# Performance work log

Hardware: AMD Instinct MI355X
Metric: run time of the kernel (lower is better)

## Reference

```python
import jax, jax.numpy as jnp
import numpy as np

TS = 0.1
ECNUM = 1024
CA1NUM = 1024
CA3NUM = 1024
CA3SIGMA = 5.0
TRACKLEN = 100
ACTNUM = 2
BS = 8192
CUELOC = int(0.1 * TRACKLEN)  # sensory cue injected at this step
NOISE_P = 0.04 * TS           # per-step EC3 spontaneous-spike probability


def _xavier_std(fan_in, fan_out):
    return float(np.sqrt(2.0 / (fan_in + fan_out)))


def setup_inputs() -> dict:
    key = jax.random.key(0)
    ks = jax.random.split(key, 6)
    cue = jax.random.normal(ks[0], (BS, ECNUM), jnp.float32)
    ec5_init = jax.random.uniform(ks[1], (BS, ECNUM), jnp.float32)
    wca3ca1 = jax.random.uniform(ks[2], (CA3NUM, CA1NUM), jnp.float32) * 0.01
    wec3ca1 = jax.random.normal(ks[3], (ECNUM, CA1NUM), jnp.float32) * _xavier_std(ECNUM, CA1NUM)
    wca1ec5 = jax.random.normal(ks[4], (CA1NUM, ECNUM), jnp.float32) * _xavier_std(CA1NUM, ECNUM)
    wca1act = jax.random.normal(ks[5], (CA1NUM, ACTNUM), jnp.float32) * _xavier_std(CA1NUM, ACTNUM)
    ca1bias = jnp.zeros((CA1NUM,), jnp.float32)
    ec5bias = jnp.zeros((ECNUM,), jnp.float32)
    actbias = jnp.zeros((ACTNUM,), jnp.float32)
    return {"cue": cue, "ec5_init": ec5_init, "wca3ca1": wca3ca1,
            "wec3ca1": wec3ca1, "wca1ec5": wca1ec5, "wca1act": wca1act,
            "ca1bias": ca1bias, "ec5bias": ec5bias, "actbias": actbias}


def _forward(cue, ec5_init, wca3ca1, wec3ca1, wca1ec5, wca1act, ca1bias, ec5bias, actbias):
    bs = cue.shape[0]
    dt = cue.dtype
    # CA3 place-cell tuning curves for all positions: (T, ca3num)
    ca3center = jnp.linspace(0.0, TRACKLEN, CA3NUM).astype(dt)
    xs = jnp.arange(TRACKLEN)
    ca3_all = jnp.exp(-((ca3center[None, :] - xs[:, None].astype(dt)) ** 2)
                      / (2.0 * CA3SIGMA ** 2))
    drive = ca3_all @ wca3ca1            # (T, ca1num), precomputed CA3->CA1 drive
    cue_mask = (xs == CUELOC).astype(dt)  # (T,)
    noise_key = jax.random.key(42)

    ec3_0 = jnp.zeros((bs, ECNUM), dt)
    ca1_0 = jnp.zeros((bs, CA1NUM), dt)

    def step(carry, inp):
        ec3, ec5, _ = carry
        d, m, t = inp
        ca1 = jax.nn.relu(d[None, :] * (1.0 + jax.nn.sigmoid(ec3 @ wec3ca1)) - ca1bias)
        ec5 = ec5 + (10.0 * TS) * (ca1 @ wca1ec5) + ec5bias
        ec5 = 0.5 + 0.5 * jax.nn.sigmoid(4.0 * (ec5 - 0.5))
        ec3 = ec5 * ec3 + m * cue
        k = jax.random.fold_in(noise_key, t)
        ec3 = ec3 + 0.2 * jax.random.bernoulli(k, NOISE_P, (bs, ECNUM)).astype(dt)
        return (ec3, ec5, ca1), None

    (ec3, ec5, ca1), _ = jax.lax.scan(step, (ec3_0, ec5_init, ca1_0),
                                      (drive, cue_mask, xs))
    return ca1 @ wca1act + actbias       # (bs, actnum)


def reference(cue, ec5_init, wca3ca1, wec3ca1, wca1ec5, wca1act, ca1bias, ec5bias, actbias):
    return _forward(cue, ec5_init, wca3ca1, wec3ca1, wca1ec5, wca1act,
                    ca1bias, ec5bias, actbias)
```

## Files before the change

### kernel.cpp

```cpp
#include <hip/hip_runtime.h>
#include <stdint.h>

#define BS 8192
#define NDIM 1024
#define T_STEPS 100
#define CUE_T 10
#define BK 64
#define NKT (NDIM / BK)

typedef __attribute__((ext_vector_type(8))) short bf16x8;
typedef __attribute__((ext_vector_type(16))) float f32x16;

__device__ inline uint16_t f32_to_bf16(float f) {
    uint32_t u = __float_as_uint(f);
    uint32_t r = u + 0x7fffu + ((u >> 16) & 1u);
    return (uint16_t)(r >> 16);
}
__device__ inline float bf16_to_f32(uint16_t h) {
    return __uint_as_float(((uint32_t)h) << 16);
}

__host__ __device__ inline uint32_t rotl32_(uint32_t x, uint32_t r) {
    return (x << r) | (x >> (32u - r));
}

__host__ __device__ inline void tf2x32(uint32_t k0, uint32_t k1,
                                       uint32_t x0, uint32_t x1,
                                       uint32_t &o0, uint32_t &o1) {
    uint32_t ks2 = k0 ^ k1 ^ 0x1BD11BDAu;
    x0 += k0; x1 += k1;
#define TF_R4(a,b,c,d) \
    x0 += x1; x1 = rotl32_(x1,(a)); x1 ^= x0; \
    x0 += x1; x1 = rotl32_(x1,(b)); x1 ^= x0; \
    x0 += x1; x1 = rotl32_(x1,(c)); x1 ^= x0; \
    x0 += x1; x1 = rotl32_(x1,(d)); x1 ^= x0;
    TF_R4(13,15,26,6)  x0 += k1;  x1 += ks2 + 1u;
    TF_R4(17,29,16,24) x0 += ks2; x1 += k0 + 2u;
    TF_R4(13,15,26,6)  x0 += k0;  x1 += k1 + 3u;
    TF_R4(17,29,16,24) x0 += k1;  x1 += ks2 + 4u;
    TF_R4(13,15,26,6)  x0 += ks2; x1 += k0 + 5u;
#undef TF_R4
    o0 = x0; o1 = x1;
}

__device__ __forceinline__ void tf2x32_x4_fold(uint32_t k0, uint32_t k1,
                                               const uint32_t idx[4],
                                               uint32_t bits[4]) {
    uint32_t ks2 = k0 ^ k1 ^ 0x1BD11BDAu;
    uint32_t x0[4], x1[4];
    #pragma unroll
    for (int i = 0; i < 4; ++i) { x0[i] = k0; x1[i] = idx[i] + k1; }
#define TF4_R(rot) \
    _Pragma("unroll") \
    for (int i = 0; i < 4; ++i) { \
        x0[i] += x1[i]; x1[i] = rotl32_(x1[i], (rot)); x1[i] ^= x0[i]; }
#define TF4_K(a0, a1) \
    _Pragma("unroll") \
    for (int i = 0; i < 4; ++i) { x0[i] += (a0); x1[i] += (a1); }
    TF4_R(13) TF4_R(15) TF4_R(26) TF4_R(6)  TF4_K(k1, ks2 + 1u)
    TF4_R(17) TF4_R(29) TF4_R(16) TF4_R(24) TF4_K(ks2, k0 + 2u)
    TF4_R(13) TF4_R(15) TF4_R(26) TF4_R(6)  TF4_K(k0, k1 + 3u)
    TF4_R(17) TF4_R(29) TF4_R(16) TF4_R(24) TF4_K(k1, ks2 + 4u)
    TF4_R(13) TF4_R(15) TF4_R(26) TF4_R(6)  TF4_K(ks2, k0 + 5u)
#undef TF4_R
#undef TF4_K
    #pragma unroll
    for (int i = 0; i < 4; ++i) bits[i] = x0[i] ^ x1[i];
}

__device__ inline float sigmoidf_(float x) {
    float e = __expf(-x);
    return __builtin_amdgcn_rcpf(1.0f + e);
}

__device__ __forceinline__ void gload16(const uint16_t* g, uint16_t* l) {
    __builtin_amdgcn_global_load_lds(
        (const __attribute__((address_space(1))) void*)g,
        (__attribute__((address_space(3))) void*)l, 16, 0, 0);
}

__global__ void init_kernel(const float* __restrict__ ec5_init,
                            uint16_t* __restrict__ ec3bf,
                            uint16_t* __restrict__ ec5bf, int n) {
    int i = blockIdx.x * blockDim.x + threadIdx.x;
    if (i < n) { ec3bf[i] = 0; ec5bf[i] = f32_to_bf16(ec5_init[i]); }
}

__global__ __launch_bounds__(256) void drive_kernel(const float* __restrict__ W,
                                                    float* __restrict__ drive) {
    __shared__ float g[4][1024];
    const int t0 = blockIdx.x * 4;
    const int c = blockIdx.y * 64 + (threadIdx.x & 63);
    const int tt = threadIdx.x >> 6;
    const float stepf = 100.0f / 1023.0f;
    for (int i = threadIdx.x; i < 4096; i += 256) {
        int t_ = i >> 10, j = i & 1023;
        float d = stepf * (float)j - (float)(t0 + t_);
        g[t_][j] = expf(-(d * d) * 0.02f);
    }
    __syncthreads();
    float a = 0.f;
    for (int j = 0; j < 1024; ++j)
        a = fmaf(g[tt][j], W[(size_t)j * NDIM + c], a);
    drive[(size_t)(t0 + tt) * NDIM + c] = a;
}

__global__ __launch_bounds__(256) void wtrans_kernel(const float* __restrict__ W,
                                                     uint16_t* __restrict__ Wt) {
    __shared__ float tile[32][33];
    int k0 = blockIdx.x * 32, n0 = blockIdx.y * 32;
    int tx = threadIdx.x & 31, ty = threadIdx.x >> 5;
    #pragma unroll
    for (int i = 0; i < 32; i += 8)
        tile[ty + i][tx] = W[(size_t)(k0 + ty + i) * NDIM + n0 + tx];
    __syncthreads();
    #pragma unroll
    for (int i = 0; i < 32; i += 8)
        Wt[(size_t)(n0 + ty + i) * NDIM + k0 + tx] = f32_to_bf16(tile[tx][ty + i]);
}

template<bool NOISE>
__device__ __forceinline__ void gemm_core_t(const uint16_t* __restrict__ A,
                                            const uint16_t* __restrict__ Bt,
                                            uint16_t* As, uint16_t* Bs,
                                            f32x16 acc[2][2],
                                            uint32_t k0_, uint32_t k1_,
                                            uint32_t obase, uint64_t &mask) {
    const int tid = threadIdx.x;
    const int wid = tid >> 6, lane = tid & 63;
    const int row0 = blockIdx.x * 128, col0 = blockIdx.y * 128;
    const int srow = lane >> 3;
    const int soff = ((lane & 7) ^ srow) * 8;
    const uint16_t* aS[4]; const uint16_t* bS[4];
    #pragma unroll
    for (int i = 0; i < 4; ++i) {
        int ch = wid * 4 + i;
        aS[i] = A  + (size_t)(row0 + ch * 8 + srow) * NDIM + soff;
        bS[i] = Bt + (size_t)(col0 + ch * 8 + srow) * NDIM + soff;
    }
    const int l31 = lane & 31, l5 = lane >> 5;
    const int wr = wid >> 1, wc = wid & 1;
    int aoff[2][4], boff[2][4];
    #pragma unroll
    for (int m = 0; m < 2; ++m)
        #pragma unroll
        for (int kk = 0; kk < 4; ++kk) {
            int ar = wr * 64 + m * 32 + l31;
            aoff[m][kk] = ar * BK + ((((kk << 1) | l5) ^ (ar & 7)) << 3);
            int br = wc * 64 + m * 32 + l31;
            boff[m][kk] = br * BK + ((((kk << 1) | l5) ^ (br & 7)) << 3);
        }

    #pragma unroll
    for (int i = 0; i < 4; ++i) {
        int ch = wid * 4 + i;
        gload16(aS[i], As + ch * 512);
        gload16(bS[i], Bs + ch * 512);
    }

    for (int kt = 0; kt < NKT; ++kt) {
        const int cur = kt & 1;
        if (kt + 1 < NKT) {
            const int nb = (cur ^ 1) * 8192;
            const int k0n = (kt + 1) * BK;
            #pragma unroll
            for (int i = 0; i < 4; ++i) {
                int ch = wid * 4 + i;
                gload16(aS[i] + k0n, As + nb + ch * 512);
                gload16(bS[i] + k0n, Bs + nb + ch * 512);
            }
            asm volatile("s_waitcnt vmcnt(8)" ::: "memory");
        } else {
            asm volatile("s_waitcnt vmcnt(0)" ::: "memory");
        }
        __builtin_amdgcn_s_barrier();
        __builtin_amdgcn_sched_barrier(0);
        const uint16_t* as = As + cur * 8192;
        const uint16_t* bs = Bs + cur * 8192;
        bf16x8 af[2][4], bfr[2][4];
        #pragma unroll
        for (int m = 0; m < 2; ++m)
            #pragma unroll
            for (int kk = 0; kk < 4; ++kk) {
                af[m][kk]  = *(const bf16x8*)&as[aoff[m][kk]];
                bfr[m][kk] = *(const bf16x8*)&bs[boff[m][kk]];
            }
        #pragma unroll
        for (int kk = 0; kk < 4; ++kk)
            #pragma unroll
            for (int m = 0; m < 2; ++m)
                #pragma unroll
                for (int n = 0; n < 2; ++n)
                    acc[m][n] = __builtin_amdgcn_mfma_f32_32x32x16_bf16(
                        af[m][kk], bfr[n][kk], acc[m][n], 0, 0, 0);
        if (NOISE) {
            uint32_t idx[4], bits[4];
            const uint32_t base = obase + (uint32_t)((kt >> 1) << 14)
                                + (uint32_t)((kt & 1) << 2);
            #pragma unroll
            for (int u = 0; u < 4; ++u) idx[u] = base + u;
            tf2x32_x4_fold(k0_, k1_, idx, bits);
            #pragma unroll
            for (int u = 0; u < 4; ++u) {
                float uu = __uint_as_float((bits[u] >> 9) | 0x3f800000u) - 1.0f;
                mask |= (uint64_t)(uu < 0.004f ? 1u : 0u) << ((kt << 2) + u);
            }
        }
        __builtin_amdgcn_sched_barrier(0);
        __builtin_amdgcn_s_barrier();
    }
}

__device__ __forceinline__ void acc_to_lds(float* lacc, f32x16 acc[2][2]) {
    const int tid = threadIdx.x, wid = tid >> 6, lane = tid & 63;
    const int wr = wid >> 1, wc = wid & 1, l31 = lane & 31, l5 = lane >> 5;
    #pragma unroll
    for (int m = 0; m < 2; ++m)
        #pragma unroll
        for (int n = 0; n < 2; ++n) {
            int c = wc * 64 + n * 32 + l31;
            int chunk = c >> 2, cj = c & 3;
            #pragma unroll
            for (int e = 0; e < 16; ++e) {
                int r = wr * 64 + m * 32 + (e & 3) + ((e >> 2) << 3) + (l5 << 2);
                lacc[r * 128 + ((chunk ^ (r & 31)) << 2) + cj] = acc[m][n][e];
            }
        }
}

__device__ __forceinline__ void acc_read8(const float* lacc, int r, int a,
                                          float4 &v0, float4 &v1) {
    int rb = r & 31;
    v0 = *(const float4*)&lacc[r * 128 + ((((a << 1) | 0) ^ rb) << 2)];
    v1 = *(const float4*)&lacc[r * 128 + ((((a << 1) | 1) ^ rb) << 2)];
}

__global__ __launch_bounds__(256, 2) void gemm1_kernel(
    const uint16_t* __restrict__ ec3bf, const uint16_t* __restrict__ W1t,
    const float* __restrict__ drv, const float* __restrict__ bias,
    uint16_t* __restrict__ ca1bf, float* __restrict__ ca1f, int writef32,
    uint64_t* __restrict__ maskbuf, uint32_t k0_, uint32_t k1_)
{
    __shared__ __align__(16) uint16_t SM[2][16384];
    uint16_t* As = SM[0];
    uint16_t* Bs = SM[1];
    f32x16 acc[2][2];
    #pragma unroll
    for (int m = 0; m < 2; ++m)
        #pragma unroll
        for (int n = 0; n < 2; ++n)
            acc[m][n] = (f32x16)(0.0f);

    const int tid = threadIdx.x;
    const int row0 = blockIdx.x * 128, col0 = blockIdx.y * 128;
    const int a = tid & 15;
    const uint32_t obase = (uint32_t)(row0 + (tid >> 4)) * NDIM
                         + (uint32_t)(col0 + a * 8);
    uint64_t mask = 0;
    gemm_core_t<true>(ec3bf, W1t, As, Bs, acc, k0_, k1_, obase, mask);

    maskbuf[(size_t)(blockIdx.y * 64 + blockIdx.x) * 256 + tid] = mask;

    float* lacc = (float*)SM;
    acc_to_lds(lacc, acc);
    __syncthreads();

    #pragma unroll
    for (int i = 0; i < 8; ++i) {
        int r = (tid >> 4) + i * 16;
        float4 v0, v1;
        acc_read8(lacc, r, a, v0, v1);
        int gc = col0 + a * 8;
        float4 d0 = *(const float4*)&drv[gc];
        float4 d1 = *(const float4*)&drv[gc + 4];
        float4 b0 = *(const float4*)&bias[gc];
        float4 b1 = *(const float4*)&bias[gc + 4];
        size_t off = (size_t)(row0 + r) * NDIM + gc;
        float vout[8];
        #pragma unroll
        for (int j = 0; j < 8; ++j) {
            float accv = j < 4 ? v0[j] : v1[j - 4];
            float dv = j < 4 ? d0[j] : d1[j - 4];
            float bi = j < 4 ? b0[j] : b1[j - 4];
            float s = sigmoidf_(accv);
            float v = dv * (1.0f + s) - bi;
            vout[j] = v > 0.0f ? v : 0.0f;
        }
        bf16x8 pk;
        #pragma unroll
        for (int j = 0; j < 8; ++j) pk[j] = (short)f32_to_bf16(vout[j]);
        *(bf16x8*)&ca1bf[off] = pk;
        if (writef32) {
            float4 f0 = {vout[0], vout[1], vout[2], vout[3]};
            float4 f1 = {vout[4], vout[5], vout[6], vout[7]};
            *(float4*)&ca1f[off] = f0;
            *(float4*)&ca1f[off + 4] = f1;
        }
    }
}

__global__ __launch_bounds__(256, 2) void gemm2_kernel(
    const uint16_t* __restrict__ ca1bf, const uint16_t* __restrict__ W2t,
    const float* __restrict__ cue, const float* __restrict__ bias,
    uint16_t* __restrict__ ec3bf, uint16_t* __restrict__ ec5bf,
    const uint64_t* __restrict__ maskbuf, int inject)
{
    __shared__ __align__(16) uint16_t SM[2][16384];
    uint16_t* As = SM[0];
    uint16_t* Bs = SM[1];
    f32x16 acc[2][2];
    #pragma unroll
    for (int m = 0; m < 2; ++m)
        #pragma unroll
        for (int n = 0; n < 2; ++n)
            acc[m][n] = (f32x16)(0.0f);

    const int tid = threadIdx.x;
    const int row0 = blockIdx.x * 128, col0 = blockIdx.y * 128;
    const int a = tid & 15;
    const uint64_t mask = maskbuf[(size_t)(blockIdx.y * 64 + blockIdx.x) * 256 + tid];

    uint64_t dummy = 0;
    gemm_core_t<false>(ca1bf, W2t, As, Bs, acc, 0u, 0u, 0u, dummy);

    bf16x8 e3v[8], e5v[8];
    #pragma unroll
    for (int i = 0; i < 8; ++i) {
        size_t off = (size_t)(row0 + (tid >> 4) + i * 16) * NDIM + col0 + a * 8;
        e3v[i] = *(const bf16x8*)&ec3bf[off];
        e5v[i] = *(const bf16x8*)&ec5bf[off];
    }

    float* lacc = (float*)SM;
    acc_to_lds(lacc, acc);
    __syncthreads();

    #pragma unroll
    for (int i = 0; i < 8; ++i) {
        int r = (tid >> 4) + i * 16;
        float4 v0, v1;
        acc_read8(lacc, r, a, v0, v1);
        int gc = col0 + a * 8;
        size_t off = (size_t)(row0 + r) * NDIM + gc;
        float4 b0 = *(const float4*)&bias[gc];
        float4 b1 = *(const float4*)&bias[gc + 4];
        float4 c0 = {0.f,0.f,0.f,0.f}, c1 = {0.f,0.f,0.f,0.f};
        if (inject) {
            c0 = *(const float4*)&cue[off];
            c1 = *(const float4*)&cue[off + 4];
        }
        bf16x8 p3, p5;
        #pragma unroll
        for (int j = 0; j < 8; ++j) {
            float accv = j < 4 ? v0[j] : v1[j - 4];
            float bi = j < 4 ? b0[j] : b1[j - 4];
            float e5 = bf16_to_f32((uint16_t)e5v[i][j]);
            float e3 = bf16_to_f32((uint16_t)e3v[i][j]);
            float u = e5 + accv + bi;
            float e5n = 0.5f + 0.5f * sigmoidf_(4.0f * (u - 0.5f));
            float e3n = e5n * e3;
            if (inject) e3n += (j < 4 ? c0[j] : c1[j - 4]);
            e3n += ((mask >> (i * 8 + j)) & 1ull) ? 0.2f : 0.0f;
            p5[j] = (short)f32_to_bf16(e5n);
            p3[j] = (short)f32_to_bf16(e3n);
        }
        *(bf16x8*)&ec5bf[off] = p5;
        *(bf16x8*)&ec3bf[off] = p3;
    }
}

__global__ __launch_bounds__(256) void final_kernel(
    const float* __restrict__ ca1,
    const float* __restrict__ wact,
    const float* __restrict__ actbias,
    float* __restrict__ out)
{
    int wave = threadIdx.x >> 6, lane = threadIdx.x & 63;
    int b = blockIdx.x * 4 + wave;
    double a0 = 0.0, a1 = 0.0;
    for (int c = lane; c < NDIM; c += 64) {
        double v = (double)ca1[(size_t)b * NDIM + c];
        a0 += v * (double)wact[c * 2 + 0];
        a1 += v * (double)wact[c * 2 + 1];
    }
    #pragma unroll
    for (int off = 32; off > 0; off >>= 1) {
        a0 += __shfl_down(a0, off);
        a1 += __shfl_down(a1, off);
    }
    if (lane == 0) {
        out[(size_t)b * 2 + 0] = (float)(a0 + (double)actbias[0]);
        out[(size_t)b * 2 + 1] = (float)(a1 + (double)actbias[1]);
    }
}

extern "C" void kernel_launch(void* const* d_in, const int* in_sizes, int n_in,
                              void* d_out, int out_size, void* d_ws, size_t ws_size,
                              hipStream_t stream) {
    const float* cue      = (const float*)d_in[0];
    const float* ec5_init = (const float*)d_in[1];
    const float* wca3ca1  = (const float*)d_in[2];
    const float* wec3ca1  = (const float*)d_in[3];
    const float* wca1ec5  = (const float*)d_in[4];
    const float* wca1act  = (const float*)d_in[5];
    const float* ca1bias  = (const float*)d_in[6];
    const float* ec5bias  = (const float*)d_in[7];
    const float* actbias  = (const float*)d_in[8];
    float* out = (float*)d_out;

    const size_t NE = (size_t)BS * NDIM;
    char* p = (char*)d_ws;
    float*    ca1f    = (float*)p;    p += NE * 4;
    uint16_t* ec3bf   = (uint16_t*)p; p += NE * 2;
    uint16_t* ec5bf   = (uint16_t*)p; p += NE * 2;
    uint16_t* ca1bf   = (uint16_t*)p; p += NE * 2;
    uint16_t* W1t     = (uint16_t*)p; p += (size_t)NDIM * NDIM * 2;
    uint16_t* W2t     = (uint16_t*)p; p += (size_t)NDIM * NDIM * 2;
    uint64_t* maskbuf = (uint64_t*)p; p += (size_t)512 * 256 * 8;
    float*    drive   = (float*)p;

    const int n = (int)NE;
    hipLaunchKernelGGL(init_kernel, dim3((n + 255) / 256), dim3(256), 0, stream,
                       ec5_init, ec3bf, ec5bf, n);
    hipLaunchKernelGGL(drive_kernel, dim3(25, 16), dim3(256), 0, stream,
                       wca3ca1, drive);
    hipLaunchKernelGGL(wtrans_kernel, dim3(32, 32), dim3(256), 0, stream, wec3ca1, W1t);
    hipLaunchKernelGGL(wtrans_kernel, dim3(32, 32), dim3(256), 0, stream, wca1ec5, W2t);

    dim3 blk(256);
    dim3 gg(BS / 128, NDIM / 128);
    for (int t = 0; t < T_STEPS; ++t) {
        uint32_t k0, k1;
        tf2x32(0u, 42u, 0u, (uint32_t)t, k0, k1);
        hipLaunchKernelGGL(gemm1_kernel, gg, blk, 0, stream,
                           ec3bf, W1t, drive + (size_t)t * NDIM, ca1bias,
                           ca1bf, ca1f, (t == T_STEPS - 1) ? 1 : 0,
                           maskbuf, k0, k1);
        if (t < T_STEPS - 1) {
            hipLaunchKernelGGL(gemm2_kernel, gg, blk, 0, stream,
                               ca1bf, W2t, cue, ec5bias, ec3bf, ec5bf,
                               maskbuf, (t == CUE_T) ? 1 : 0);
        }
    }
    hipLaunchKernelGGL(final_kernel, dim3(BS / 4), blk, 0, stream,
                       ca1f, wca1act, actbias, out);
}
```

Measured before the change: 6.308 ms.

## Use 512-thread blocks with 8 waves per 128x128 tile in both GEMMs

Both step GEMMs now launch 512 threads per block, so 8 waves each compute a 32x64 sub-tile instead of 4 waves each computing 64x64. This halves the accumulators and fragments held per thread, and the global-to-LDS loads and noise-mask generation are redistributed across the extra threads. The noise mask shrinks to 32 bits per thread, and drive/bias loads are hoisted out of the epilogue loops. The aim is more waves in flight to hide latency. The cost is lower MFMA reuse per wave, more LDS fragment reads per MFMA, and more contention at the block barriers.

Measured after the change: 6.559 ms. 4.0% more time.

```diff
diff --git a/kernel.cpp b/kernel.cpp
--- a/kernel.cpp
+++ b/kernel.cpp
@@ -123,53 +123,49 @@
 __device__ __forceinline__ void gemm_core_t(const uint16_t* __restrict__ A,
                                             const uint16_t* __restrict__ Bt,
                                             uint16_t* As, uint16_t* Bs,
-                                            f32x16 acc[2][2],
+                                            f32x16 acc[2],
                                             uint32_t k0_, uint32_t k1_,
-                                            uint32_t obase, uint64_t &mask) {
+                                            uint32_t obase, uint32_t &mask) {
     const int tid = threadIdx.x;
     const int wid = tid >> 6, lane = tid & 63;
     const int row0 = blockIdx.x * 128, col0 = blockIdx.y * 128;
-    const int srow = lane >> 3;
-    const int soff = ((lane & 7) ^ srow) * 8;
-    const uint16_t* aS[4]; const uint16_t* bS[4];
-    #pragma unroll
-    for (int i = 0; i < 4; ++i) {
-        int ch = wid * 4 + i;
-        aS[i] = A  + (size_t)(row0 + ch * 8 + srow) * NDIM + soff;
-        bS[i] = Bt + (size_t)(col0 + ch * 8 + srow) * NDIM + soff;
-    }
+    const int ch0 = tid, ch1 = tid + 512;
+    const int r0c = ch0 >> 3, r1c = ch1 >> 3;
+    const int s0 = ((ch0 & 7) ^ (r0c & 7)) << 3;
+    const int s1 = ((ch1 & 7) ^ (r1c & 7)) << 3;
+    const uint16_t* aS0 = A  + (size_t)(row0 + r0c) * NDIM + s0;
+    const uint16_t* aS1 = A  + (size_t)(row0 + r1c) * NDIM + s1;
+    const uint16_t* bS0 = Bt + (size_t)(col0 + r0c) * NDIM + s0;
+    const uint16_t* bS1 = Bt + (size_t)(col0 + r1c) * NDIM + s1;
     const int l31 = lane & 31, l5 = lane >> 5;
     const int wr = wid >> 1, wc = wid & 1;
-    int aoff[2][4], boff[2][4];
-    #pragma unroll
-    for (int m = 0; m < 2; ++m)
-        #pragma unroll
-        for (int kk = 0; kk < 4; ++kk) {
-            int ar = wr * 64 + m * 32 + l31;
-            aoff[m][kk] = ar * BK + ((((kk << 1) | l5) ^ (ar & 7)) << 3);
-            int br = wc * 64 + m * 32 + l31;
-            boff[m][kk] = br * BK + ((((kk << 1) | l5) ^ (br & 7)) << 3);
-        }
-
-    #pragma unroll
-    for (int i = 0; i < 4; ++i) {
-        int ch = wid * 4 + i;
-        gload16(aS[i], As + ch * 512);
-        gload16(bS[i], Bs + ch * 512);
-    }
+    const int ar = wr * 32 + l31;
+    int aoff[4], boff[2][4];
+    #pragma unroll
+    for (int kk = 0; kk < 4; ++kk) {
+        aoff[kk] = ar * BK + ((((kk << 1) | l5) ^ (ar & 7)) << 3);
+        #pragma unroll
+        for (int n = 0; n < 2; ++n) {
+            int br = wc * 64 + n * 32 + l31;
+            boff[n][kk] = br * BK + ((((kk << 1) | l5) ^ (br & 7)) << 3);
+        }
+    }
+
+    gload16(aS0, As + ch0 * 8);
+    gload16(aS1, As + ch1 * 8);
+    gload16(bS0, Bs + ch0 * 8);
+    gload16(bS1, Bs + ch1 * 8);
 
     for (int kt = 0; kt < NKT; ++kt) {
         const int cur = kt & 1;
         if (kt + 1 < NKT) {
             const int nb = (cur ^ 1) * 8192;
             const int k0n = (kt + 1) * BK;
-            #pragma unroll
-            for (int i = 0; i < 4; ++i) {
-                int ch = wid * 4 + i;
-                gload16(aS[i] + k0n, As + nb + ch * 512);
-                gload16(bS[i] + k0n, Bs + nb + ch * 512);
-            }
-            asm volatile("s_waitcnt vmcnt(8)" ::: "memory");
+            gload16(aS0 + k0n, As + nb + ch0 * 8);
+            gload16(aS1 + k0n, As + nb + ch1 * 8);
+            gload16(bS0 + k0n, Bs + nb + ch0 * 8);
+            gload16(bS1 + k0n, Bs + nb + ch1 * 8);
+            asm volatile("s_waitcnt vmcnt(4)" ::: "memory");
         } else {
             asm volatile("s_waitcnt vmcnt(0)" ::: "memory");
         }
@@ -177,33 +173,32 @@
         __builtin_amdgcn_sched_barrier(0);
         const uint16_t* as = As + cur * 8192;
         const uint16_t* bs = Bs + cur * 8192;
-        bf16x8 af[2][4], bfr[2][4];
-        #pragma unroll
-        for (int m = 0; m < 2; ++m)
+        bf16x8 af[4], bfr[2][4];
+        #pragma unroll
+        for (int kk = 0; kk < 4; ++kk) {
+            af[kk] = *(const bf16x8*)&as[aoff[kk]];
             #pragma unroll
-            for (int kk = 0; kk < 4; ++kk) {
-                af[m][kk]  = *(const bf16x8*)&as[aoff[m][kk]];
-                bfr[m][kk] = *(const bf16x8*)&bs[boff[m][kk]];
-            }
+            for (int n = 0; n < 2; ++n)
+                bfr[n][kk] = *(const bf16x8*)&bs[boff[n][kk]];
+        }
         #pragma unroll
         for (int kk = 0; kk < 4; ++kk)
             #pragma unroll
-            for (int m = 0; m < 2; ++m)
-                #pragma unroll
-                for (int n = 0; n < 2; ++n)
-                    acc[m][n] = __builtin_amdgcn_mfma_f32_32x32x16_bf16(
-                        af[m][kk], bfr[n][kk], acc[m][n], 0, 0, 0);
-        if (NOISE) {
+            for (int n = 0; n < 2; ++n)
+                acc[n] = __builtin_amdgcn_mfma_f32_32x32x16_bf16(
+                    af[kk], bfr[n][kk], acc[n], 0, 0, 0);
+        if (NOISE && !(kt & 1)) {
             uint32_t idx[4], bits[4];
-            const uint32_t base = obase + (uint32_t)((kt >> 1) << 14)
-                                + (uint32_t)((kt & 1) << 2);
             #pragma unroll
-            for (int u = 0; u < 4; ++u) idx[u] = base + u;
+            for (int u = 0; u < 4; ++u) {
+                int e = (kt << 1) + u;
+                idx[u] = obase + (uint32_t)((e >> 3) << 15) + (uint32_t)(e & 7);
+            }
             tf2x32_x4_fold(k0_, k1_, idx, bits);
             #pragma unroll
             for (int u = 0; u < 4; ++u) {
                 float uu = __uint_as_float((bits[u] >> 9) | 0x3f800000u) - 1.0f;
-                mask |= (uint64_t)(uu < 0.004f ? 1u : 0u) << ((kt << 2) + u);
+                mask |= (uint32_t)(uu < 0.004f ? 1u : 0u) << ((kt << 1) + u);
             }
         }
         __builtin_amdgcn_sched_barrier(0);
@@ -211,21 +206,19 @@
     }
 }
 
-__device__ __forceinline__ void acc_to_lds(float* lacc, f32x16 acc[2][2]) {
+__device__ __forceinline__ void acc_to_lds(float* lacc, f32x16 acc[2]) {
     const int tid = threadIdx.x, wid = tid >> 6, lane = tid & 63;
     const int wr = wid >> 1, wc = wid & 1, l31 = lane & 31, l5 = lane >> 5;
     #pragma unroll
-    for (int m = 0; m < 2; ++m)
-        #pragma unroll
-        for (int n = 0; n < 2; ++n) {
-            int c = wc * 64 + n * 32 + l31;
-            int chunk = c >> 2, cj = c & 3;
-            #pragma unroll
-            for (int e = 0; e < 16; ++e) {
-                int r = wr * 64 + m * 32 + (e & 3) + ((e >> 2) << 3) + (l5 << 2);
-                lacc[r * 128 + ((chunk ^ (r & 31)) << 2) + cj] = acc[m][n][e];
-            }
-        }
+    for (int n = 0; n < 2; ++n) {
+        int c = wc * 64 + n * 32 + l31;
+        int chunk = c >> 2, cj = c & 3;
+        #pragma unroll
+        for (int e = 0; e < 16; ++e) {
+            int r = wr * 32 + (e & 3) + ((e >> 2) << 3) + (l5 << 2);
+            lacc[r * 128 + ((chunk ^ (r & 31)) << 2) + cj] = acc[n][e];
+        }
+    }
 }
 
 __device__ __forceinline__ void acc_read8(const float* lacc, int r, int a,
@@ -235,46 +228,43 @@
     v1 = *(const float4*)&lacc[r * 128 + ((((a << 1) | 1) ^ rb) << 2)];
 }
 
-__global__ __launch_bounds__(256, 2) void gemm1_kernel(
+__global__ __launch_bounds__(512, 4) void gemm1_kernel(
     const uint16_t* __restrict__ ec3bf, const uint16_t* __restrict__ W1t,
     const float* __restrict__ drv, const float* __restrict__ bias,
     uint16_t* __restrict__ ca1bf, float* __restrict__ ca1f, int writef32,
-    uint64_t* __restrict__ maskbuf, uint32_t k0_, uint32_t k1_)
+    uint32_t* __restrict__ maskbuf, uint32_t k0_, uint32_t k1_)
 {
     __shared__ __align__(16) uint16_t SM[2][16384];
     uint16_t* As = SM[0];
     uint16_t* Bs = SM[1];
-    f32x16 acc[2][2];
-    #pragma unroll
-    for (int m = 0; m < 2; ++m)
-        #pragma unroll
-        for (int n = 0; n < 2; ++n)
-            acc[m][n] = (f32x16)(0.0f);
+    f32x16 acc[2];
+    acc[0] = (f32x16)(0.0f);
+    acc[1] = (f32x16)(0.0f);
 
     const int tid = threadIdx.x;
     const int row0 = blockIdx.x * 128, col0 = blockIdx.y * 128;
     const int a = tid & 15;
     const uint32_t obase = (uint32_t)(row0 + (tid >> 4)) * NDIM
                          + (uint32_t)(col0 + a * 8);
-    uint64_t mask = 0;
+    uint32_t mask = 0;
     gemm_core_t<true>(ec3bf, W1t, As, Bs, acc, k0_, k1_, obase, mask);
 
-    maskbuf[(size_t)(blockIdx.y * 64 + blockIdx.x) * 256 + tid] = mask;
+    maskbuf[(size_t)(blockIdx.y * 64 + blockIdx.x) * 512 + tid] = mask;
 
     float* lacc = (float*)SM;
     acc_to_lds(lacc, acc);
     __syncthreads();
 
-    #pragma unroll
-    for (int i = 0; i < 8; ++i) {
-        int r = (tid >> 4) + i * 16;
+    int gc = col0 + a * 8;
+    float4 d0 = *(const float4*)&drv[gc];
+    float4 d1 = *(const float4*)&drv[gc + 4];
+    float4 b0 = *(const float4*)&bias[gc];
+    float4 b1 = *(const float4*)&bias[gc + 4];
+    #pragma unroll
+    for (int i = 0; i < 4; ++i) {
+        int r = (tid >> 4) + i * 32;
         float4 v0, v1;
         acc_read8(lacc, r, a, v0, v1);
-        int gc = col0 + a * 8;
-        float4 d0 = *(const float4*)&drv[gc];
-        float4 d1 = *(const float4*)&drv[gc + 4];
-        float4 b0 = *(const float4*)&bias[gc];
-        float4 b1 = *(const float4*)&bias[gc + 4];
         size_t off = (size_t)(row0 + r) * NDIM + gc;
         float vout[8];
         #pragma unroll
@@ -299,34 +289,31 @@
     }
 }
 
-__global__ __launch_bounds__(256, 2) void gemm2_kernel(
+__global__ __launch_bounds__(512, 4) void gemm2_kernel(
     const uint16_t* __restrict__ ca1bf, const uint16_t* __restrict__ W2t,
     const float* __restrict__ cue, const float* __restrict__ bias,
     uint16_t* __restrict__ ec3bf, uint16_t* __restrict__ ec5bf,
-    const uint64_t* __restrict__ maskbuf, int inject)
+    const uint32_t* __restrict__ maskbuf, int inject)
 {
     __shared__ __align__(16) uint16_t SM[2][16384];
     uint16_t* As = SM[0];
     uint16_t* Bs = SM[1];
-    f32x16 acc[2][2];
-    #pragma unroll
-    for (int m = 0; m < 2; ++m)
-        #pragma unroll
-        for (int n = 0; n < 2; ++n)
-            acc[m][n] = (f32x16)(0.0f);
+    f32x16 acc[2];
+    acc[0] = (f32x16)(0.0f);
+    acc[1] = (f32x16)(0.0f);
 
     const int tid = threadIdx.x;
     const int row0 = blockIdx.x * 128, col0 = blockIdx.y * 128;
     const int a = tid & 15;
-    const uint64_t mask = maskbuf[(size_t)(blockIdx.y * 64 + blockIdx.x) * 256 + tid];
-
-    uint64_t dummy = 0;
+    const uint32_t mask = maskbuf[(size_t)(blockIdx.y * 64 + blockIdx.x) * 512 + tid];
+
+    uint32_t dummy = 0;
     gemm_core_t<false>(ca1bf, W2t, As, Bs, acc, 0u, 0u, 0u, dummy);
 
-    bf16x8 e3v[8], e5v[8];
-    #pragma unroll
-    for (int i = 0; i < 8; ++i) {
-        size_t off = (size_t)(row0 + (tid >> 4) + i * 16) * NDIM + col0 + a * 8;
+    bf16x8 e3v[4], e5v[4];
+    #pragma unroll
+    for (int i = 0; i < 4; ++i) {
+        size_t off = (size_t)(row0 + (tid >> 4) + i * 32) * NDIM + col0 + a * 8;
         e3v[i] = *(const bf16x8*)&ec3bf[off];
         e5v[i] = *(const bf16x8*)&ec5bf[off];
     }
@@ -335,15 +322,15 @@
     acc_to_lds(lacc, acc);
     __syncthreads();
 
-    #pragma unroll
-    for (int i = 0; i < 8; ++i) {
-        int r = (tid >> 4) + i * 16;
+    int gc = col0 + a * 8;
+    float4 b0 = *(const float4*)&bias[gc];
+    float4 b1 = *(const float4*)&bias[gc + 4];
+    #pragma unroll
+    for (int i = 0; i < 4; ++i) {
+        int r = (tid >> 4) + i * 32;
         float4 v0, v1;
         acc_read8(lacc, r, a, v0, v1);
-        int gc = col0 + a * 8;
         size_t off = (size_t)(row0 + r) * NDIM + gc;
-        float4 b0 = *(const float4*)&bias[gc];
-        float4 b1 = *(const float4*)&bias[gc + 4];
         float4 c0 = {0.f,0.f,0.f,0.f}, c1 = {0.f,0.f,0.f,0.f};
         if (inject) {
             c0 = *(const float4*)&cue[off];
@@ -360,7 +347,7 @@
             float e5n = 0.5f + 0.5f * sigmoidf_(4.0f * (u - 0.5f));
             float e3n = e5n * e3;
             if (inject) e3n += (j < 4 ? c0[j] : c1[j - 4]);
-            e3n += ((mask >> (i * 8 + j)) & 1ull) ? 0.2f : 0.0f;
+            e3n += ((mask >> (i * 8 + j)) & 1u) ? 0.2f : 0.0f;
             p5[j] = (short)f32_to_bf16(e5n);
             p3[j] = (short)f32_to_bf16(e3n);
         }
@@ -416,7 +403,7 @@
     uint16_t* ca1bf   = (uint16_t*)p; p += NE * 2;
     uint16_t* W1t     = (uint16_t*)p; p += (size_t)NDIM * NDIM * 2;
     uint16_t* W2t     = (uint16_t*)p; p += (size_t)NDIM * NDIM * 2;
-    uint64_t* maskbuf = (uint64_t*)p; p += (size_t)512 * 256 * 8;
+    uint32_t* maskbuf = (uint32_t*)p; p += (size_t)512 * 512 * 4;
     float*    drive   = (float*)p;
 
     const int n = (int)NE;
@@ -427,7 +414,7 @@
     hipLaunchKernelGGL(wtrans_kernel, dim3(32, 32), dim3(256), 0, stream, wec3ca1, W1t);
     hipLaunchKernelGGL(wtrans_kernel, dim3(32, 32), dim3(256), 0, stream, wca1ec5, W2t);
 
-    dim3 blk(256);
+    dim3 blk(512);
     dim3 gg(BS / 128, NDIM / 128);
     for (int t = 0; t < T_STEPS; ++t) {
         uint32_t k0, k1;
@@ -442,6 +429,6 @@
                                maskbuf, (t == CUE_T) ? 1 : 0);
         }
     }
-    hipLaunchKernelGGL(final_kernel, dim3(BS / 4), blk, 0, stream,
+    hipLaunchKernelGGL(final_kernel, dim3(BS / 4), dim3(256), 0, stream,
                        ca1f, wca1act, actbias, out);
 }
```

## Batch noise-mask generation into a separate chunked kernel out of GEMM1

Applied to the files above, without the earlier changes.

Moves the per-step Threefry Bernoulli noise-mask generation out of the GEMM1 main loop into a standalone kernel that precomputes masks for up to 20 timesteps per launch. GEMM2 reads the mask slot for the current step from a larger ring buffer. The aim is to take integer hash ALU work off the MFMA-bound GEMM loop and run it as one wide launch. The cost is an extra launch every 20 steps plus more mask memory traffic. Drive and bias loads in the epilogues are also hoisted out of the row loop.

Result: slower. 6.602 ms (+4.7%).

```diff
diff --git a/kernel.cpp b/kernel.cpp
--- a/kernel.cpp
+++ b/kernel.cpp
@@ -7,6 +7,8 @@
 #define CUE_T 10
 #define BK 64
 #define NKT (NDIM / BK)
+#define MASK_CHUNK 20
+#define SLOTS_PER_STEP (512 * 256)
 
 typedef __attribute__((ext_vector_type(8))) short bf16x8;
 typedef __attribute__((ext_vector_type(16))) float f32x16;
@@ -86,6 +88,34 @@
     if (i < n) { ec3bf[i] = 0; ec5bf[i] = f32_to_bf16(ec5_init[i]); }
 }
 
+__global__ __launch_bounds__(256) void noise_kernel(uint64_t* __restrict__ maskbuf,
+                                                    int tbase) {
+    const int tid = threadIdx.x;
+    const int lin = blockIdx.x;
+    const int stp = tbase + blockIdx.y;
+    uint32_t k0, k1;
+    tf2x32(0u, 42u, 0u, (uint32_t)stp, k0, k1);
+    const int gx = lin & 63, gy = lin >> 6;
+    const uint32_t obase = (uint32_t)(gx * 128 + (tid >> 4)) * NDIM
+                         + (uint32_t)(gy * 128 + (tid & 15) * 8);
+    uint64_t mask = 0;
+    #pragma unroll
+    for (int b = 0; b < 16; ++b) {
+        uint32_t idx[4], bits[4];
+        const uint32_t base = obase + (uint32_t)((b >> 1) << 14)
+                            + (uint32_t)((b & 1) << 2);
+        #pragma unroll
+        for (int u = 0; u < 4; ++u) idx[u] = base + u;
+        tf2x32_x4_fold(k0, k1, idx, bits);
+        #pragma unroll
+        for (int u = 0; u < 4; ++u) {
+            float uu = __uint_as_float((bits[u] >> 9) | 0x3f800000u) - 1.0f;
+            mask |= (uint64_t)(uu < 0.004f ? 1u : 0u) << ((b << 2) + u);
+        }
+    }
+    maskbuf[(size_t)blockIdx.y * SLOTS_PER_STEP + (size_t)lin * 256 + tid] = mask;
+}
+
 __global__ __launch_bounds__(256) void drive_kernel(const float* __restrict__ W,
                                                     float* __restrict__ drive) {
     __shared__ float g[4][1024];
@@ -119,13 +149,10 @@
         Wt[(size_t)(n0 + ty + i) * NDIM + k0 + tx] = f32_to_bf16(tile[tx][ty + i]);
 }
 
-template<bool NOISE>
-__device__ __forceinline__ void gemm_core_t(const uint16_t* __restrict__ A,
-                                            const uint16_t* __restrict__ Bt,
-                                            uint16_t* As, uint16_t* Bs,
-                                            f32x16 acc[2][2],
-                                            uint32_t k0_, uint32_t k1_,
-                                            uint32_t obase, uint64_t &mask) {
+__device__ __forceinline__ void gemm_core(const uint16_t* __restrict__ A,
+                                          const uint16_t* __restrict__ Bt,
+                                          uint16_t* As, uint16_t* Bs,
+                                          f32x16 acc[2][2]) {
     const int tid = threadIdx.x;
     const int wid = tid >> 6, lane = tid & 63;
     const int row0 = blockIdx.x * 128, col0 = blockIdx.y * 128;
@@ -193,19 +220,6 @@
                 for (int n = 0; n < 2; ++n)
                     acc[m][n] = __builtin_amdgcn_mfma_f32_32x32x16_bf16(
                         af[m][kk], bfr[n][kk], acc[m][n], 0, 0, 0);
-        if (NOISE) {
-            uint32_t idx[4], bits[4];
-            const uint32_t base = obase + (uint32_t)((kt >> 1) << 14)
-                                + (uint32_t)((kt & 1) << 2);
-            #pragma unroll
-            for (int u = 0; u < 4; ++u) idx[u] = base + u;
-            tf2x32_x4_fold(k0_, k1_, idx, bits);
-            #pragma unroll
-            for (int u = 0; u < 4; ++u) {
-                float uu = __uint_as_float((bits[u] >> 9) | 0x3f800000u) - 1.0f;
-                mask |= (uint64_t)(uu < 0.004f ? 1u : 0u) << ((kt << 2) + u);
-            }
-        }
         __builtin_amdgcn_sched_barrier(0);
         __builtin_amdgcn_s_barrier();
     }
@@ -238,8 +252,7 @@
 __global__ __launch_bounds__(256, 2) void gemm1_kernel(
     const uint16_t* __restrict__ ec3bf, const uint16_t* __restrict__ W1t,
     const float* __restrict__ drv, const float* __restrict__ bias,
-    uint16_t* __restrict__ ca1bf, float* __restrict__ ca1f, int writef32,
-    uint64_t* __restrict__ maskbuf, uint32_t k0_, uint32_t k1_)
+    uint16_t* __restrict__ ca1bf, float* __restrict__ ca1f, int writef32)
 {
     __shared__ __align__(16) uint16_t SM[2][16384];
     uint16_t* As = SM[0];
@@ -250,31 +263,25 @@
         #pragma unroll
         for (int n = 0; n < 2; ++n)
             acc[m][n] = (f32x16)(0.0f);
+    gemm_core(ec3bf, W1t, As, Bs, acc);
+
+    float* lacc = (float*)SM;
+    acc_to_lds(lacc, acc);
+    __syncthreads();
 
     const int tid = threadIdx.x;
     const int row0 = blockIdx.x * 128, col0 = blockIdx.y * 128;
     const int a = tid & 15;
-    const uint32_t obase = (uint32_t)(row0 + (tid >> 4)) * NDIM
-                         + (uint32_t)(col0 + a * 8);
-    uint64_t mask = 0;
-    gemm_core_t<true>(ec3bf, W1t, As, Bs, acc, k0_, k1_, obase, mask);
-
-    maskbuf[(size_t)(blockIdx.y * 64 + blockIdx.x) * 256 + tid] = mask;
-
-    float* lacc = (float*)SM;
-    acc_to_lds(lacc, acc);
-    __syncthreads();
-
+    int gc = col0 + a * 8;
+    float4 d0 = *(const float4*)&drv[gc];
+    float4 d1 = *(const float4*)&drv[gc + 4];
+    float4 b0 = *(const float4*)&bias[gc];
+    float4 b1 = *(const float4*)&bias[gc + 4];
     #pragma unroll
     for (int i = 0; i < 8; ++i) {
         int r = (tid >> 4) + i * 16;
         float4 v0, v1;
         acc_read8(lacc, r, a, v0, v1);
-        int gc = col0 + a * 8;
-        float4 d0 = *(const float4*)&drv[gc];
-        float4 d1 = *(const float4*)&drv[gc + 4];
-        float4 b0 = *(const float4*)&bias[gc];
-        float4 b1 = *(const float4*)&bias[gc + 4];
         size_t off = (size_t)(row0 + r) * NDIM + gc;
         float vout[8];
         #pragma unroll
@@ -303,7 +310,7 @@
     const uint16_t* __restrict__ ca1bf, const uint16_t* __restrict__ W2t,
     const float* __restrict__ cue, const float* __restrict__ bias,
     uint16_t* __restrict__ ec3bf, uint16_t* __restrict__ ec5bf,
-    const uint64_t* __restrict__ maskbuf, int inject)
+    const uint64_t* __restrict__ maskstep, int inject)
 {
     __shared__ __align__(16) uint16_t SM[2][16384];
     uint16_t* As = SM[0];
@@ -318,10 +325,9 @@
     const int tid = threadIdx.x;
     const int row0 = blockIdx.x * 128, col0 = blockIdx.y * 128;
     const int a = tid & 15;
-    const uint64_t mask = maskbuf[(size_t)(blockIdx.y * 64 + blockIdx.x) * 256 + tid];
-
-    uint64_t dummy = 0;
-    gemm_core_t<false>(ca1bf, W2t, As, Bs, acc, 0u, 0u, 0u, dummy);
+    const uint64_t mask = maskstep[(size_t)(blockIdx.y * 64 + blockIdx.x) * 256 + tid];
+
+    gemm_core(ca1bf, W2t, As, Bs, acc);
 
     bf16x8 e3v[8], e5v[8];
     #pragma unroll
@@ -335,15 +341,15 @@
     acc_to_lds(lacc, acc);
     __syncthreads();
 
+    int gc = col0 + a * 8;
+    float4 b0 = *(const float4*)&bias[gc];
+    float4 b1 = *(const float4*)&bias[gc + 4];
     #pragma unroll
     for (int i = 0; i < 8; ++i) {
         int r = (tid >> 4) + i * 16;
         float4 v0, v1;
         acc_read8(lacc, r, a, v0, v1);
-        int gc = col0 + a * 8;
         size_t off = (size_t)(row0 + r) * NDIM + gc;
-        float4 b0 = *(const float4*)&bias[gc];
-        float4 b1 = *(const float4*)&bias[gc + 4];
         float4 c0 = {0.f,0.f,0.f,0.f}, c1 = {0.f,0.f,0.f,0.f};
         if (inject) {
             c0 = *(const float4*)&cue[off];
@@ -416,7 +422,7 @@
     uint16_t* ca1bf   = (uint16_t*)p; p += NE * 2;
     uint16_t* W1t     = (uint16_t*)p; p += (size_t)NDIM * NDIM * 2;
     uint16_t* W2t     = (uint16_t*)p; p += (size_t)NDIM * NDIM * 2;
-    uint64_t* maskbuf = (uint64_t*)p; p += (size_t)512 * 256 * 8;
+    uint64_t* maskbuf = (uint64_t*)p; p += (size_t)MASK_CHUNK * SLOTS_PER_STEP * 8;
     float*    drive   = (float*)p;
 
     const int n = (int)NE;
@@ -430,16 +436,20 @@
     dim3 blk(256);
     dim3 gg(BS / 128, NDIM / 128);
     for (int t = 0; t < T_STEPS; ++t) {
-        uint32_t k0, k1;
-        tf2x32(0u, 42u, 0u, (uint32_t)t, k0, k1);
+        if (t < T_STEPS - 1 && (t % MASK_CHUNK) == 0) {
+            int nsteps = T_STEPS - 1 - t;
+            if (nsteps > MASK_CHUNK) nsteps = MASK_CHUNK;
+            hipLaunchKernelGGL(noise_kernel, dim3(512, nsteps), blk, 0, stream,
+                               maskbuf, t);
+        }
         hipLaunchKernelGGL(gemm1_kernel, gg, blk, 0, stream,
                            ec3bf, W1t, drive + (size_t)t * NDIM, ca1bias,
-                           ca1bf, ca1f, (t == T_STEPS - 1) ? 1 : 0,
-                           maskbuf, k0, k1);
+                           ca1bf, ca1f, (t == T_STEPS - 1) ? 1 : 0);
         if (t < T_STEPS - 1) {
             hipLaunchKernelGGL(gemm2_kernel, gg, blk, 0, stream,
                                ca1bf, W2t, cue, ec5bias, ec3bf, ec5bf,
-                               maskbuf, (t == CUE_T) ? 1 : 0);
+                               maskbuf + (size_t)(t % MASK_CHUNK) * SLOTS_PER_STEP,
+                               (t == CUE_T) ? 1 : 0);
         }
     }
     hipLaunchKernelGGL(final_kernel, dim3(BS / 4), blk, 0, stream,
```

## Warp-specialize gemm1: separate noise-RNG waves from MFMA waves in 512-thread blocks

Applied to the files above, without the earlier changes.

The first GEMM kernel now launches 512 threads per block. Four waves do the tile loads and MFMA work, while four extra waves compute the Threefry bernoulli noise mask in parallel, with barriers keeping them in step. This moves the RNG integer work off the critical MFMA path, and the epilogue is spread over twice as many threads. In exchange, per-block register and occupancy pressure rises (launch bounds 512,4), and the bias/drive loads in the epilogues are hoisted out of their loops.

Result: faster. 6.175 ms (-2.1%).

```diff
diff --git a/kernel.cpp b/kernel.cpp
--- a/kernel.cpp
+++ b/kernel.cpp
@@ -119,13 +119,189 @@
         Wt[(size_t)(n0 + ty + i) * NDIM + k0 + tx] = f32_to_bf16(tile[tx][ty + i]);
 }
 
-template<bool NOISE>
-__device__ __forceinline__ void gemm_core_t(const uint16_t* __restrict__ A,
-                                            const uint16_t* __restrict__ Bt,
-                                            uint16_t* As, uint16_t* Bs,
-                                            f32x16 acc[2][2],
-                                            uint32_t k0_, uint32_t k1_,
-                                            uint32_t obase, uint64_t &mask) {
+__device__ __forceinline__ void acc_to_lds(float* lacc, f32x16 acc[2][2]) {
+    const int tid = threadIdx.x, wid = tid >> 6, lane = tid & 63;
+    const int wr = wid >> 1, wc = wid & 1, l31 = lane & 31, l5 = lane >> 5;
+    #pragma unroll
+    for (int m = 0; m < 2; ++m)
+        #pragma unroll
+        for (int n = 0; n < 2; ++n) {
+            int c = wc * 64 + n * 32 + l31;
+            int chunk = c >> 2, cj = c & 3;
+            #pragma unroll
+            for (int e = 0; e < 16; ++e) {
+                int r = wr * 64 + m * 32 + (e & 3) + ((e >> 2) << 3) + (l5 << 2);
+                lacc[r * 128 + ((chunk ^ (r & 31)) << 2) + cj] = acc[m][n][e];
+            }
+        }
+}
+
+__device__ __forceinline__ void acc_read8(const float* lacc, int r, int a,
+                                          float4 &v0, float4 &v1) {
+    int rb = r & 31;
+    v0 = *(const float4*)&lacc[r * 128 + ((((a << 1) | 0) ^ rb) << 2)];
+    v1 = *(const float4*)&lacc[r * 128 + ((((a << 1) | 1) ^ rb) << 2)];
+}
+
+__global__ __launch_bounds__(512, 4) void gemm1_kernel(
+    const uint16_t* __restrict__ ec3bf, const uint16_t* __restrict__ W1t,
+    const float* __restrict__ drv, const float* __restrict__ bias,
+    uint16_t* __restrict__ ca1bf, float* __restrict__ ca1f, int writef32,
+    uint64_t* __restrict__ maskbuf, uint32_t k0_, uint32_t k1_)
+{
+    __shared__ __align__(16) uint16_t SM[2][16384];
+    uint16_t* As = SM[0];
+    uint16_t* Bs = SM[1];
+    const int tid = threadIdx.x;
+    const int wid = tid >> 6, lane = tid & 63;
+    const bool gw = wid < 4;
+    const int row0 = blockIdx.x * 128, col0 = blockIdx.y * 128;
+
+    f32x16 acc[2][2];
+    #pragma unroll
+    for (int m = 0; m < 2; ++m)
+        #pragma unroll
+        for (int n = 0; n < 2; ++n)
+            acc[m][n] = (f32x16)(0.0f);
+
+    const int srow = lane >> 3;
+    const int soff = ((lane & 7) ^ srow) * 8;
+    const int gwid = wid & 3;
+    const uint16_t* aS[4]; const uint16_t* bS[4];
+    #pragma unroll
+    for (int i = 0; i < 4; ++i) {
+        int ch = gwid * 4 + i;
+        aS[i] = ec3bf + (size_t)(row0 + ch * 8 + srow) * NDIM + soff;
+        bS[i] = W1t   + (size_t)(col0 + ch * 8 + srow) * NDIM + soff;
+    }
+    const int l31 = lane & 31, l5 = lane >> 5;
+    const int wr = gwid >> 1, wc = gwid & 1;
+    int aoff[2][4], boff[2][4];
+    #pragma unroll
+    for (int m = 0; m < 2; ++m)
+        #pragma unroll
+        for (int kk = 0; kk < 4; ++kk) {
+            int ar = wr * 64 + m * 32 + l31;
+            aoff[m][kk] = ar * BK + ((((kk << 1) | l5) ^ (ar & 7)) << 3);
+            int br = wc * 64 + m * 32 + l31;
+            boff[m][kk] = br * BK + ((((kk << 1) | l5) ^ (br & 7)) << 3);
+        }
+
+    const int nt = tid & 255;
+    const uint32_t obase = (uint32_t)(row0 + (nt >> 4)) * NDIM
+                         + (uint32_t)(col0 + (nt & 15) * 8);
+    uint64_t mask = 0;
+
+    if (gw) {
+        #pragma unroll
+        for (int i = 0; i < 4; ++i) {
+            int ch = gwid * 4 + i;
+            gload16(aS[i], As + ch * 512);
+            gload16(bS[i], Bs + ch * 512);
+        }
+    }
+
+    for (int kt = 0; kt < NKT; ++kt) {
+        const int cur = kt & 1;
+        if (gw) {
+            if (kt + 1 < NKT) {
+                const int nb = (cur ^ 1) * 8192;
+                const int k0n = (kt + 1) * BK;
+                #pragma unroll
+                for (int i = 0; i < 4; ++i) {
+                    int ch = gwid * 4 + i;
+                    gload16(aS[i] + k0n, As + nb + ch * 512);
+                    gload16(bS[i] + k0n, Bs + nb + ch * 512);
+                }
+                asm volatile("s_waitcnt vmcnt(8)" ::: "memory");
+            } else {
+                asm volatile("s_waitcnt vmcnt(0)" ::: "memory");
+            }
+        }
+        __builtin_amdgcn_s_barrier();
+        __builtin_amdgcn_sched_barrier(0);
+        if (gw) {
+            const uint16_t* as = As + cur * 8192;
+            const uint16_t* bs = Bs + cur * 8192;
+            bf16x8 af[2][4], bfr[2][4];
+            #pragma unroll
+            for (int m = 0; m < 2; ++m)
+                #pragma unroll
+                for (int kk = 0; kk < 4; ++kk) {
+                    af[m][kk]  = *(const bf16x8*)&as[aoff[m][kk]];
+                    bfr[m][kk] = *(const bf16x8*)&bs[boff[m][kk]];
+                }
+            #pragma unroll
+            for (int kk = 0; kk < 4; ++kk)
+                #pragma unroll
+                for (int m = 0; m < 2; ++m)
+                    #pragma unroll
+                    for (int n = 0; n < 2; ++n)
+                        acc[m][n] = __builtin_amdgcn_mfma_f32_32x32x16_bf16(
+                            af[m][kk], bfr[n][kk], acc[m][n], 0, 0, 0);
+        } else {
+            uint32_t idx[4], bits[4];
+            const uint32_t base = obase + (uint32_t)((kt >> 1) << 14)
+                                + (uint32_t)((kt & 1) << 2);
+            #pragma unroll
+            for (int u = 0; u < 4; ++u) idx[u] = base + u;
+            tf2x32_x4_fold(k0_, k1_, idx, bits);
+            #pragma unroll
+            for (int u = 0; u < 4; ++u) {
+                float uu = __uint_as_float((bits[u] >> 9) | 0x3f800000u) - 1.0f;
+                mask |= (uint64_t)(uu < 0.004f ? 1u : 0u) << ((kt << 2) + u);
+            }
+        }
+        __builtin_amdgcn_sched_barrier(0);
+        __builtin_amdgcn_s_barrier();
+    }
+
+    if (!gw)
+        maskbuf[(size_t)(blockIdx.y * 64 + blockIdx.x) * 256 + nt] = mask;
+
+    float* lacc = (float*)SM;
+    if (gw) acc_to_lds(lacc, acc);
+    __syncthreads();
+
+    const int a = tid & 15;
+    int gc = col0 + a * 8;
+    float4 d0 = *(const float4*)&drv[gc];
+    float4 d1 = *(const float4*)&drv[gc + 4];
+    float4 b0 = *(const float4*)&bias[gc];
+    float4 b1 = *(const float4*)&bias[gc + 4];
+    #pragma unroll
+    for (int i = 0; i < 4; ++i) {
+        int r = (tid >> 4) + i * 32;
+        float4 v0, v1;
+        acc_read8(lacc, r, a, v0, v1);
+        size_t off = (size_t)(row0 + r) * NDIM + gc;
+        float vout[8];
+        #pragma unroll
+        for (int j = 0; j < 8; ++j) {
+            float accv = j < 4 ? v0[j] : v1[j - 4];
+            float dv = j < 4 ? d0[j] : d1[j - 4];
+            float bi = j < 4 ? b0[j] : b1[j - 4];
+            float s = sigmoidf_(accv);
+            float v = dv * (1.0f + s) - bi;
+            vout[j] = v > 0.0f ? v : 0.0f;
+        }
+        bf16x8 pk;
+        #pragma unroll
+        for (int j = 0; j < 8; ++j) pk[j] = (short)f32_to_bf16(vout[j]);
+        *(bf16x8*)&ca1bf[off] = pk;
+        if (writef32) {
+            float4 f0 = {vout[0], vout[1], vout[2], vout[3]};
+            float4 f1 = {vout[4], vout[5], vout[6], vout[7]};
+            *(float4*)&ca1f[off] = f0;
+            *(float4*)&ca1f[off + 4] = f1;
+        }
+    }
+}
+
+__device__ __forceinline__ void gemm_core(const uint16_t* __restrict__ A,
+                                          const uint16_t* __restrict__ Bt,
+                                          uint16_t* As, uint16_t* Bs,
+                                          f32x16 acc[2][2]) {
     const int tid = threadIdx.x;
     const int wid = tid >> 6, lane = tid & 63;
     const int row0 = blockIdx.x * 128, col0 = blockIdx.y * 128;
@@ -193,109 +369,8 @@
                 for (int n = 0; n < 2; ++n)
                     acc[m][n] = __builtin_amdgcn_mfma_f32_32x32x16_bf16(
                         af[m][kk], bfr[n][kk], acc[m][n], 0, 0, 0);
-        if (NOISE) {
-            uint32_t idx[4], bits[4];
-            const uint32_t base = obase + (uint32_t)((kt >> 1) << 14)
-                                + (uint32_t)((kt & 1) << 2);
-            #pragma unroll
-            for (int u = 0; u < 4; ++u) idx[u] = base + u;
-            tf2x32_x4_fold(k0_, k1_, idx, bits);
-            #pragma unroll
-            for (int u = 0; u < 4; ++u) {
-                float uu = __uint_as_float((bits[u] >> 9) | 0x3f800000u) - 1.0f;
-                mask |= (uint64_t)(uu < 0.004f ? 1u : 0u) << ((kt << 2) + u);
-            }
-        }
         __builtin_amdgcn_sched_barrier(0);
         __builtin_amdgcn_s_barrier();
-    }
-}
-
-__device__ __forceinline__ void acc_to_lds(float* lacc, f32x16 acc[2][2]) {
-    const int tid = threadIdx.x, wid = tid >> 6, lane = tid & 63;
-    const int wr = wid >> 1, wc = wid & 1, l31 = lane & 31, l5 = lane >> 5;
-    #pragma unroll
-    for (int m = 0; m < 2; ++m)
-        #pragma unroll
-        for (int n = 0; n < 2; ++n) {
-            int c = wc * 64 + n * 32 + l31;
-            int chunk = c >> 2, cj = c & 3;
-            #pragma unroll
-            for (int e = 0; e < 16; ++e) {
-                int r = wr * 64 + m * 32 + (e & 3) + ((e >> 2) << 3) + (l5 << 2);
-                lacc[r * 128 + ((chunk ^ (r & 31)) << 2) + cj] = acc[m][n][e];
-            }
-        }
-}
-
-__device__ __forceinline__ void acc_read8(const float* lacc, int r, int a,
-                                          float4 &v0, float4 &v1) {
-    int rb = r & 31;
-    v0 = *(const float4*)&lacc[r * 128 + ((((a << 1) | 0) ^ rb) << 2)];
-    v1 = *(const float4*)&lacc[r * 128 + ((((a << 1) | 1) ^ rb) << 2)];
-}
-
-__global__ __launch_bounds__(256, 2) void gemm1_kernel(
-    const uint16_t* __restrict__ ec3bf, const uint16_t* __restrict__ W1t,
-    const float* __restrict__ drv, const float* __restrict__ bias,
-    uint16_t* __restrict__ ca1bf, float* __restrict__ ca1f, int writef32,
-    uint64_t* __restrict__ maskbuf, uint32_t k0_, uint32_t k1_)
-{
-    __shared__ __align__(16) uint16_t SM[2][16384];
-    uint16_t* As = SM[0];
-    uint16_t* Bs = SM[1];
-    f32x16 acc[2][2];
-    #pragma unroll
-    for (int m = 0; m < 2; ++m)
-        #pragma unroll
-        for (int n = 0; n < 2; ++n)
-            acc[m][n] = (f32x16)(0.0f);
-
-    const int tid = threadIdx.x;
-    const int row0 = blockIdx.x * 128, col0 = blockIdx.y * 128;
-    const int a = tid & 15;
-    const uint32_t obase = (uint32_t)(row0 + (tid >> 4)) * NDIM
-                         + (uint32_t)(col0 + a * 8);
-    uint64_t mask = 0;
-    gemm_core_t<true>(ec3bf, W1t, As, Bs, acc, k0_, k1_, obase, mask);
-
-    maskbuf[(size_t)(blockIdx.y * 64 + blockIdx.x) * 256 + tid] = mask;
-
-    float* lacc = (float*)SM;
-    acc_to_lds(lacc, acc);
-    __syncthreads();
-
-    #pragma unroll
-    for (int i = 0; i < 8; ++i) {
-        int r = (tid >> 4) + i * 16;
-        float4 v0, v1;
-        acc_read8(lacc, r, a, v0, v1);
-        int gc = col0 + a * 8;
-        float4 d0 = *(const float4*)&drv[gc];
-        float4 d1 = *(const float4*)&drv[gc + 4];
-        float4 b0 = *(const float4*)&bias[gc];
-        float4 b1 = *(const float4*)&bias[gc + 4];
-        size_t off = (size_t)(row0 + r) * NDIM + gc;
-        float vout[8];
-        #pragma unroll
-        for (int j = 0; j < 8; ++j) {
-            float accv = j < 4 ? v0[j] : v1[j - 4];
-            float dv = j < 4 ? d0[j] : d1[j - 4];
-            float bi = j < 4 ? b0[j] : b1[j - 4];
-            float s = sigmoidf_(accv);
-            float v = dv * (1.0f + s) - bi;
-            vout[j] = v > 0.0f ? v : 0.0f;
-        }
-        bf16x8 pk;
-        #pragma unroll
-        for (int j = 0; j < 8; ++j) pk[j] = (short)f32_to_bf16(vout[j]);
-        *(bf16x8*)&ca1bf[off] = pk;
-        if (writef32) {
-            float4 f0 = {vout[0], vout[1], vout[2], vout[3]};
-            float4 f1 = {vout[4], vout[5], vout[6], vout[7]};
-            *(float4*)&ca1f[off] = f0;
-            *(float4*)&ca1f[off + 4] = f1;
-        }
     }
 }
 
@@ -320,8 +395,7 @@
     const int a = tid & 15;
     const uint64_t mask = maskbuf[(size_t)(blockIdx.y * 64 + blockIdx.x) * 256 + tid];
 
-    uint64_t dummy = 0;
-    gemm_core_t<false>(ca1bf, W2t, As, Bs, acc, 0u, 0u, 0u, dummy);
+    gemm_core(ca1bf, W2t, As, Bs, acc);
 
     bf16x8 e3v[8], e5v[8];
     #pragma unroll
@@ -335,15 +409,15 @@
     acc_to_lds(lacc, acc);
     __syncthreads();
 
+    int gc = col0 + a * 8;
+    float4 b0 = *(const float4*)&bias[gc];
+    float4 b1 = *(const float4*)&bias[gc + 4];
     #pragma unroll
     for (int i = 0; i < 8; ++i) {
         int r = (tid >> 4) + i * 16;
         float4 v0, v1;
         acc_read8(lacc, r, a, v0, v1);
-        int gc = col0 + a * 8;
         size_t off = (size_t)(row0 + r) * NDIM + gc;
-        float4 b0 = *(const float4*)&bias[gc];
-        float4 b1 = *(const float4*)&bias[gc + 4];
         float4 c0 = {0.f,0.f,0.f,0.f}, c1 = {0.f,0.f,0.f,0.f};
         if (inject) {
             c0 = *(const float4*)&cue[off];
@@ -427,21 +501,20 @@
     hipLaunchKernelGGL(wtrans_kernel, dim3(32, 32), dim3(256), 0, stream, wec3ca1, W1t);
     hipLaunchKernelGGL(wtrans_kernel, dim3(32, 32), dim3(256), 0, stream, wca1ec5, W2t);
 
-    dim3 blk(256);
     dim3 gg(BS / 128, NDIM / 128);
     for (int t = 0; t < T_STEPS; ++t) {
         uint32_t k0, k1;
         tf2x32(0u, 42u, 0u, (uint32_t)t, k0, k1);
-        hipLaunchKernelGGL(gemm1_kernel, gg, blk, 0, stream,
+        hipLaunchKernelGGL(gemm1_kernel, gg, dim3(512), 0, stream,
                            ec3bf, W1t, drive + (size_t)t * NDIM, ca1bias,
                            ca1bf, ca1f, (t == T_STEPS - 1) ? 1 : 0,
                            maskbuf, k0, k1);
         if (t < T_STEPS - 1) {
-            hipLaunchKernelGGL(gemm2_kernel, gg, blk, 0, stream,
+            hipLaunchKernelGGL(gemm2_kernel, gg, dim3(256), 0, stream,
                                ca1bf, W2t, cue, ec5bias, ec3bf, ec5bf,
                                maskbuf, (t == CUE_T) ? 1 : 0);
         }
     }
-    hipLaunchKernelGGL(final_kernel, dim3(BS / 4), blk, 0, stream,
+    hipLaunchKernelGGL(final_kernel, dim3(BS / 4), dim3(256), 0, stream,
                        ca1f, wca1act, actbias, out);
 }
```
